# Kernel tuning notes

Measured on AMD Instinct MI355X. Metric: run time of the kernel, lower is better.

Reference implementation:

```python
import jax, jax.numpy as jnp
import numpy as np

D = 2        # NUM_DIM (spatial/velocity dimension)
B = 64       # number of (r, r') query pairs
P = 512      # num coefficient positions
NV = 64      # num velocity quadrature points
NC = 1       # num coefficient channels (sigma)
H = 64       # attention MLP hidden width
TW = 128     # transport MLP width
DEPTH = 3    # res_block_depth


def setup_inputs() -> dict:
    key = jax.random.key(0)
    ks = jax.random.split(key, 20)
    rnd = lambda i, shape, s=1.0: (s * jax.random.normal(ks[i], shape, dtype=jnp.float32))
    uni = lambda i, shape: jax.random.uniform(ks[i], shape, dtype=jnp.float32)
    return dict(
        coords=rnd(0, (B, 2 * D)),
        coords_prime=rnd(1, (B, 2 * D)),
        scattering_kernel=uni(2, (B, NV)),
        position_coords=rnd(3, (P, D)),
        sigma=uni(4, (P, NC)),
        velocity_coords=rnd(5, (NV, D)),
        velocity_weights=uni(6, (NV,)),
        self_scattering_kernel=uni(7, (NV, NV)),
        aW0=rnd(8, (2 * D + 2, H), (2 * D + 2) ** -0.5), ab0=jnp.zeros((H,), jnp.float32),
        aW1=rnd(9, (H, H), H ** -0.5), ab1=jnp.zeros((H,), jnp.float32),
        aW2=rnd(10, (H, 1), H ** -0.5), ab2=jnp.zeros((1,), jnp.float32),
        tW0=rnd(11, (4 * D + NC, TW), (4 * D + NC) ** -0.5), tb0=jnp.zeros((TW,), jnp.float32),
        tW1=rnd(12, (TW, TW), TW ** -0.5), tb1=jnp.zeros((TW,), jnp.float32),
        tW2=rnd(13, (TW, TW), TW ** -0.5), tb2=jnp.zeros((TW,), jnp.float32),
        rW=rnd(14, (DEPTH - 1, TW, TW), TW ** -0.5), rb=jnp.zeros((DEPTH - 1, TW), jnp.float32),
        fW=rnd(15, (TW, 1), TW ** -0.5), fb=jnp.zeros((1,), jnp.float32),
    )


def _coeff(x, v, pos, vals, aW0, ab0, aW1, ab1, aW2, ab2):
    # x, v: (..., D); pos: (P, D); vals: (P, NC)
    coords = jnp.concatenate([x, v], axis=-1)                          # (..., 2D)
    ang_g = v / jnp.sqrt(jnp.sum(v * v, axis=-1, keepdims=True) + 1e-16)
    rel = x[..., None, :] - pos                                        # (..., P, D)
    rd = jnp.sqrt(jnp.sum(rel * rel, axis=-1) + 1e-16)                 # (..., P)
    pl = jnp.einsum('...pd,...d->...p', rel, ang_g)                    # positions_local
    al = pl / (rd + 1e-8)                                              # angles_local
    frames = jnp.stack([al, pl], axis=-1)                              # (..., P, 2)
    q = jnp.broadcast_to(coords[..., None, :], frames.shape[:-1] + (coords.shape[-1],))
    qk = jnp.concatenate([q, frames], axis=-1)                         # (..., P, 2D+2)
    h = jax.nn.relu(qk @ aW0 + ab0)
    h = jax.nn.relu(h @ aW1 + ab1)
    logits = (h @ aW2 + ab2)[..., 0]                                   # (..., P)
    logits = jnp.where(pl > 0, logits, -1e30)
    attw = jax.nn.softmax(logits, axis=-1)
    attn = jnp.einsum('...p,pc->...c', attw, vals)                     # (..., NC)
    return jnp.exp(-attn)


def _transport(x, v, xp, vp, pos, vals,
               aW0, ab0, aW1, ab1, aW2, ab2, tW0, tb0, tW1, tb1, tW2, tb2):
    coeff = _coeff(x, v, pos, vals, aW0, ab0, aW1, ab1, aW2, ab2)
    inp = jnp.concatenate([x, v, xp, vp, coeff], axis=-1)              # (..., 4D+NC)
    h = jax.nn.relu(inp @ tW0 + tb0)
    h = jax.nn.relu(h @ tW1 + tb1)
    h = jax.nn.relu(h @ tW2 + tb2)                                     # activate_final=True
    return jnp.exp(h)                                                  # (..., TW)


def _forward(coords, coords_prime, scattering_kernel, position_coords, sigma,
             velocity_coords, velocity_weights, self_scattering_kernel,
             aW0, ab0, aW1, ab1, aW2, ab2, tW0, tb0, tW1, tb1, tW2, tb2,
             rW, rb, fW, fb):
    x, v = coords[:, :D], coords[:, D:]
    xp, vp = coords_prime[:, :D], coords_prime[:, D:]
    mlp_p = (aW0, ab0, aW1, ab1, aW2, ab2, tW0, tb0, tW1, tb1, tW2, tb2)
    # direct transport term: (B, TW)
    g = _transport(x, v, xp, vp, position_coords, sigma, *mlp_p)
    # scatter model: vmap over velocity_coords -> (B, NV, TW)
    b = coords.shape[0]
    vB = jnp.broadcast_to(velocity_coords, (b, NV, D))
    xB = jnp.broadcast_to(x[:, None, :], (b, NV, D))
    xpB = jnp.broadcast_to(xp[:, None, :], (b, NV, D))
    vpB = jnp.broadcast_to(vp[:, None, :], (b, NV, D))
    cur = _transport(xB, vB, xpB, vpB, position_coords, sigma, *mlp_p)
    res_w = (1.0 - self_scattering_kernel) * velocity_weights          # (NV, NV)
    outs = [cur]
    for l in range(DEPTH - 1):  # layer_stack with per-layer params
        r = jnp.einsum('ij,bjw->biw', res_w, cur)
        r = jax.nn.relu(r @ rW[l] + rb[l])                             # MLP([TW]), activate_final
        cur = cur + r
        outs.append(cur)
    scat = jnp.stack(outs)                                             # (DEPTH, B, NV, TW)
    w = (1.0 - scattering_kernel) * velocity_weights                   # (B, NV)
    g = g + jnp.einsum('bj,dbjw->bw', w, scat)
    return g @ fW + fb                                                 # (B, 1)


def reference(coords, coords_prime, scattering_kernel, position_coords, sigma,
              velocity_coords, velocity_weights, self_scattering_kernel,
              aW0, ab0, aW1, ab1, aW2, ab2, tW0, tb0, tW1, tb1, tW2, tb2,
              rW, rb, fW, fb):
    return _forward(coords, coords_prime, scattering_kernel, position_coords, sigma,
                    velocity_coords, velocity_weights, self_scattering_kernel,
                    aW0, ab0, aW1, ab1, aW2, ab2, tW0, tb0, tW1, tb1, tW2, tb2,
                    rW, rb, fW, fb)
```

## Files before the change

kernel.cpp:

```cpp
#include <hip/hip_runtime.h>
#include <hip/hip_bf16.h>
#include <math.h>

#define D 2
#define B 64
#define P 512
#define NV 64
#define H 64
#define TW 128
#define NQ (B*NV + B)

typedef short short8 __attribute__((ext_vector_type(8)));
typedef short short4v __attribute__((ext_vector_type(4)));
typedef float f32x4 __attribute__((ext_vector_type(4)));
typedef int   int4v  __attribute__((ext_vector_type(4)));

static __device__ __forceinline__ unsigned short f2bf(float f) {
    unsigned int u = __builtin_bit_cast(unsigned int, f);
    u += 0x7FFFu + ((u >> 16) & 1u);
    return (unsigned short)(u >> 16);
}
static __device__ __forceinline__ unsigned int pk2bf(float a, float b) {
    __hip_bfloat162 h = __float22bfloat162_rn(make_float2(a, b));
    unsigned int u;
    __builtin_memcpy(&u, &h, 4);
    return u;
}

__global__ __launch_bounds__(256, 2) void coeff_kernel(
    const float* __restrict__ coords, const float* __restrict__ vel,
    const float* __restrict__ pos, const float* __restrict__ sigma,
    const float* __restrict__ aW0, const float* __restrict__ ab0,
    const float* __restrict__ aW1, const float* __restrict__ ab1,
    const float* __restrict__ aW2, const float* __restrict__ ab2,
    float* __restrict__ coeff_out)
{
    __shared__ unsigned short s_w1t[64*72];
    __shared__ float2 s_pos[P];
    __shared__ float  s_logit[2*P];

    const int tid  = threadIdx.x;
    const int lane = tid & 63, wid = tid >> 6;
    const int l15 = lane & 15, lg = lane >> 4;
    const int qi   = wid >> 1;
    const int half = wid & 1;
    const int q = blockIdx.x*2 + qi;

    for (int i = tid; i < H*H; i += 256) {
        const int k = i >> 6, n = i & 63;
        s_w1t[n*72 + k] = f2bf(aW1[i]);
    }
    {
        const float4 p4 = ((const float4*)pos)[tid];
        *(float4*)&s_pos[tid*2] = p4;
    }

    float x0, x1, v0, v1;
    {
        int b;
        if (q < B*NV) { b = q >> 6; const int j = q & 63;
            v0 = vel[2*j]; v1 = vel[2*j+1];
        } else { b = q - B*NV;
            v0 = coords[4*b+2]; v1 = coords[4*b+3];
        }
        x0 = coords[4*b]; x1 = coords[4*b+1];
    }
    const float rinv = rsqrtf(v0*v0 + v1*v1 + 1e-16f);
    const float a0 = v0*rinv, a1 = v1*rinv;

    float basev[16], w4v[16], w5v[16];
    #pragma unroll
    for (int jj = 0; jj < 16; ++jj) {
        const int k = lg*8 + (jj & 7) + (jj >> 3)*32;
        basev[jj] = ab0[k] + x0*aW0[k] + x1*aW0[64+k] + v0*aW0[128+k] + v1*aW0[192+k];
        w4v[jj]   = aW0[256+k];
        w5v[jj]   = aW0[320+k];
    }

    f32x4 b1v[4], w2v[4];
    #pragma unroll
    for (int nt = 0; nt < 4; ++nt) {
        const int n0 = nt*16 + lg*4;
        b1v[nt] = *(const f32x4*)&ab1[n0];
        w2v[nt] = *(const f32x4*)&aW2[n0];
    }
    __syncthreads();

    short8 afrag[4][2];
    #pragma unroll
    for (int nt = 0; nt < 4; ++nt)
        #pragma unroll
        for (int ks = 0; ks < 2; ++ks)
            afrag[nt][ks] = *(const short8*)&s_w1t[(nt*16 + l15)*72 + ks*32 + lg*8];

    #pragma unroll
    for (int jj = 0; jj < 16; ++jj)
        asm volatile("" : "+v"(basev[jj]), "+v"(w4v[jj]), "+v"(w5v[jj]));
    #pragma unroll
    for (int nt = 0; nt < 4; ++nt)
        asm volatile("" : "+v"(b1v[nt]), "+v"(w2v[nt]),
                          "+v"(afrag[nt][0]), "+v"(afrag[nt][1]));

    float2 pxy = s_pos[half*256 + l15];
    for (int ps = 0; ps < 16; ++ps) {
        const int prow = half*256 + ps*16 + l15;
        const float2 nxt = (ps < 15) ? s_pos[prow + 16] : pxy;

        const float rx = x0 - pxy.x;
        const float ry = x1 - pxy.y;
        const float rd = __builtin_amdgcn_sqrtf(rx*rx + ry*ry + 1e-16f);
        const float pl = rx*a0 + ry*a1;
        const float al = __fdividef(pl, rd + 1e-8f);

        int4v wlo, whi;
        #pragma unroll
        for (int jp = 0; jp < 4; ++jp) {
            const float t0 = fmaxf(fmaf(pl, w5v[2*jp],   fmaf(al, w4v[2*jp],   basev[2*jp])),   0.f);
            const float t1 = fmaxf(fmaf(pl, w5v[2*jp+1], fmaf(al, w4v[2*jp+1], basev[2*jp+1])), 0.f);
            const float u0 = fmaxf(fmaf(pl, w5v[8+2*jp],   fmaf(al, w4v[8+2*jp],   basev[8+2*jp])),   0.f);
            const float u1 = fmaxf(fmaf(pl, w5v[8+2*jp+1], fmaf(al, w4v[8+2*jp+1], basev[8+2*jp+1])), 0.f);
            wlo[jp] = (int)pk2bf(t0, t1);
            whi[jp] = (int)pk2bf(u0, u1);
        }
        const short8 bf0 = __builtin_bit_cast(short8, wlo);
        const short8 bf1 = __builtin_bit_cast(short8, whi);

        float ssum = 0.f;
        #pragma unroll
        for (int nt = 0; nt < 4; ++nt) {
            f32x4 acc = b1v[nt];
            acc = __builtin_amdgcn_mfma_f32_16x16x32_bf16(afrag[nt][0], bf0, acc, 0, 0, 0);
            acc = __builtin_amdgcn_mfma_f32_16x16x32_bf16(afrag[nt][1], bf1, acc, 0, 0, 0);
            ssum += fmaxf(acc[0], 0.f) * w2v[nt][0];
            ssum += fmaxf(acc[1], 0.f) * w2v[nt][1];
            ssum += fmaxf(acc[2], 0.f) * w2v[nt][2];
            ssum += fmaxf(acc[3], 0.f) * w2v[nt][3];
        }
        ssum += __shfl_xor(ssum, 16, 64);
        ssum += __shfl_xor(ssum, 32, 64);
        if (lane < 16) s_logit[qi*512 + prow] = (pl > 0.f) ? ssum : -1e30f;
        pxy = nxt;
    }
    __syncthreads();

    const float* lgb = &s_logit[qi*512];
    const float4 l0 = *(const float4*)&lgb[lane*8];
    const float4 l1 = *(const float4*)&lgb[lane*8 + 4];
    float m = fmaxf(fmaxf(fmaxf(l0.x, l0.y), fmaxf(l0.z, l0.w)),
                    fmaxf(fmaxf(l1.x, l1.y), fmaxf(l1.z, l1.w)));
    #pragma unroll
    for (int o = 32; o > 0; o >>= 1) m = fmaxf(m, __shfl_xor(m, o, 64));

    const float4 g0 = *(const float4*)&sigma[lane*8];
    const float4 g1 = *(const float4*)&sigma[lane*8 + 4];
    float S = 0.f, T = 0.f, e;
    e = __expf(l0.x - m); S += e; T += e*g0.x;
    e = __expf(l0.y - m); S += e; T += e*g0.y;
    e = __expf(l0.z - m); S += e; T += e*g0.z;
    e = __expf(l0.w - m); S += e; T += e*g0.w;
    e = __expf(l1.x - m); S += e; T += e*g1.x;
    e = __expf(l1.y - m); S += e; T += e*g1.y;
    e = __expf(l1.z - m); S += e; T += e*g1.z;
    e = __expf(l1.w - m); S += e; T += e*g1.w;
    #pragma unroll
    for (int o = 32; o > 0; o >>= 1) { S += __shfl_xor(S, o, 64); T += __shfl_xor(T, o, 64); }
    if (lane == 0 && half == 0) coeff_out[q] = __expf(-(T / S));
}

__global__ __launch_bounds__(128) void transport_kernel(
    const float* __restrict__ coords, const float* __restrict__ coordsp,
    const float* __restrict__ vel,
    const float* __restrict__ tW0, const float* __restrict__ tb0,
    const float* __restrict__ tW1, const float* __restrict__ tb1,
    const float* __restrict__ tW2, const float* __restrict__ tb2,
    const float* __restrict__ coeff_ws, float* __restrict__ cur_ws,
    float* __restrict__ g_ws)
{
    __shared__ float sh[TW];
    const int t = threadIdx.x, q = blockIdx.x;
    float in2, in3;
    int b;
    if (q < B*NV) { b = q >> 6; const int j = q & 63;
        in2 = vel[2*j]; in3 = vel[2*j+1];
    } else { b = q - B*NV;
        in2 = coords[4*b+2]; in3 = coords[4*b+3];
    }
    const float in0 = coords[4*b],  in1 = coords[4*b+1];
    const float p0 = coordsp[4*b],  p1 = coordsp[4*b+1];
    const float p2 = coordsp[4*b+2], p3 = coordsp[4*b+3];
    const float cf = coeff_ws[q];

    float h = tb0[t]
        + in0*tW0[t]       + in1*tW0[TW+t]   + in2*tW0[2*TW+t] + in3*tW0[3*TW+t]
        + p0 *tW0[4*TW+t]  + p1 *tW0[5*TW+t] + p2 *tW0[6*TW+t] + p3 *tW0[7*TW+t]
        + cf *tW0[8*TW+t];
    h = fmaxf(h, 0.f);
    sh[t] = h; __syncthreads();

    float h2 = tb1[t];
    for (int i = 0; i < TW; ++i) h2 += sh[i]*tW1[i*TW+t];
    h2 = fmaxf(h2, 0.f);
    __syncthreads(); sh[t] = h2; __syncthreads();

    float h3 = tb2[t];
    for (int i = 0; i < TW; ++i) h3 += sh[i]*tW2[i*TW+t];
    h3 = fmaxf(h3, 0.f);
    const float o = expf(h3);

    if (q < B*NV) cur_ws[q*TW + t] = o;
    else          g_ws[(q - B*NV)*TW + t] = o;
}

__global__ __launch_bounds__(512) void scatter_kernel(
    const float* __restrict__ scat_k, const float* __restrict__ vw,
    const float* __restrict__ ssk,
    const float* __restrict__ rW, const float* __restrict__ rb,
    const float* __restrict__ fW, const float* __restrict__ fb,
    const float* __restrict__ cur_ws, const float* __restrict__ g_ws,
    float* __restrict__ out)
{
    __shared__ unsigned short s_At[128*72];
    __shared__ unsigned short s_r[64*136];
    __shared__ unsigned short s_rWt[128*136];
    __shared__ float s_wl[NV];
    __shared__ float s_fin[4*128];
    __shared__ float s_red[2];

    const int tid = threadIdx.x, b = blockIdx.x;
    const int lane = tid & 63, wid = tid >> 6;
    const int wm = wid & 3, wn = wid >> 2;
    const int l15 = lane & 15, lg = lane >> 4;
    const int irow = wm*16 + lg*4;

    if (tid < NV) s_wl[tid] = (1.f - scat_k[b*NV + tid]) * vw[tid];

    {
        const int w = tid & 127, j0 = tid >> 7;
        #pragma unroll
        for (int k = 0; k < 16; ++k) {
            const int j = j0 + 4*k;
            s_At[w*72 + j] = f2bf(cur_ws[(b*NV + j)*TW + w]);
        }
    }

    float areg[4][4], sreg[4][4];
    #pragma unroll
    for (int n = 0; n < 4; ++n) {
        const int wcol = wn*64 + n*16 + l15;
        #pragma unroll
        for (int rg = 0; rg < 4; ++rg) {
            const float v = cur_ws[(b*NV + irow + rg)*TW + wcol];
            areg[n][rg] = v; sreg[n][rg] = v;
        }
    }

    for (int l = 0; l < 2; ++l) {
        {
            const float* rWl = rW + l*TW*TW;
            const int w = tid & 127, u0 = (tid >> 7)*4;
            #pragma unroll
            for (int k = 0; k < 8; ++k) {
                const int u = u0 + 16*k;
                short4v pk;
                #pragma unroll
                for (int c = 0; c < 4; ++c) pk[c] = (short)f2bf(rWl[(u+c)*TW + w]);
                *(short4v*)&s_rWt[w*136 + u] = pk;
            }
        }
        __syncthreads();

        {
            short8 afrag[2];
            const int row = wm*16 + l15;
            #pragma unroll
            for (int ks = 0; ks < 2; ++ks) {
                const int k0 = ks*32 + lg*8;
                #pragma unroll
                for (int j = 0; j < 8; ++j) {
                    const float rv = (1.f - ssk[row*NV + k0 + j]) * vw[k0 + j];
                    afrag[ks][j] = (short)f2bf(rv);
                }
            }
            #pragma unroll
            for (int n = 0; n < 4; ++n) {
                const int col = wn*64 + n*16 + l15;
                f32x4 acc = {0.f, 0.f, 0.f, 0.f};
                #pragma unroll
                for (int ks = 0; ks < 2; ++ks) {
                    const short8 bfr = *(const short8*)&s_At[col*72 + ks*32 + lg*8];
                    acc = __builtin_amdgcn_mfma_f32_16x16x32_bf16(afrag[ks], bfr, acc, 0, 0, 0);
                }
                #pragma unroll
                for (int rg = 0; rg < 4; ++rg)
                    s_r[(irow + rg)*136 + col] = f2bf(acc[rg]);
            }
        }
        __syncthreads();

        {
            short8 af2[4];
            #pragma unroll
            for (int ks = 0; ks < 4; ++ks)
                af2[ks] = *(const short8*)&s_r[(wm*16 + l15)*136 + ks*32 + lg*8];
            #pragma unroll
            for (int n = 0; n < 4; ++n) {
                const int col = wn*64 + n*16 + l15;
                f32x4 acc = {0.f, 0.f, 0.f, 0.f};
                #pragma unroll
                for (int ks = 0; ks < 4; ++ks) {
                    const short8 bfr = *(const short8*)&s_rWt[col*136 + ks*32 + lg*8];
                    acc = __builtin_amdgcn_mfma_f32_16x16x32_bf16(af2[ks], bfr, acc, 0, 0, 0);
                }
                const float rbv = rb[l*TW + col];
                short4v pk;
                #pragma unroll
                for (int rg = 0; rg < 4; ++rg) {
                    areg[n][rg] += fmaxf(acc[rg] + rbv, 0.f);
                    sreg[n][rg] += areg[n][rg];
                    pk[rg] = (short)f2bf(areg[n][rg]);
                }
                *(short4v*)&s_At[col*72 + irow] = pk;
            }
        }
        __syncthreads();
    }

    float p[4];
    #pragma unroll
    for (int n = 0; n < 4; ++n) {
        float acc = 0.f;
        #pragma unroll
        for (int rg = 0; rg < 4; ++rg) acc += s_wl[irow + rg] * sreg[n][rg];
        acc += __shfl_xor(acc, 16, 64);
        acc += __shfl_xor(acc, 32, 64);
        p[n] = acc;
    }
    if (lg == 0) {
        #pragma unroll
        for (int n = 0; n < 4; ++n)
            s_fin[wm*128 + wn*64 + n*16 + l15] = p[n];
    }
    __syncthreads();

    if (tid < 128) {
        const int w = tid;
        const float tot = s_fin[w] + s_fin[128 + w] + s_fin[256 + w] + s_fin[384 + w];
        float pw = (g_ws[b*TW + w] + tot) * fW[w];
        #pragma unroll
        for (int o = 32; o > 0; o >>= 1) pw += __shfl_down(pw, o, 64);
        if ((tid & 63) == 0) s_red[tid >> 6] = pw;
    }
    __syncthreads();
    if (tid == 0) out[b] = s_red[0] + s_red[1] + fb[0];
}

extern "C" void kernel_launch(void* const* d_in, const int* in_sizes, int n_in,
                              void* d_out, int out_size, void* d_ws, size_t ws_size,
                              hipStream_t stream) {
    const float* coords  = (const float*)d_in[0];
    const float* coordsp = (const float*)d_in[1];
    const float* scatk   = (const float*)d_in[2];
    const float* pos     = (const float*)d_in[3];
    const float* sigma   = (const float*)d_in[4];
    const float* vel     = (const float*)d_in[5];
    const float* vw      = (const float*)d_in[6];
    const float* ssk     = (const float*)d_in[7];
    const float* aW0 = (const float*)d_in[8];
    const float* ab0 = (const float*)d_in[9];
    const float* aW1 = (const float*)d_in[10];
    const float* ab1 = (const float*)d_in[11];
    const float* aW2 = (const float*)d_in[12];
    const float* ab2 = (const float*)d_in[13];
    const float* tW0 = (const float*)d_in[14];
    const float* tb0 = (const float*)d_in[15];
    const float* tW1 = (const float*)d_in[16];
    const float* tb1 = (const float*)d_in[17];
    const float* tW2 = (const float*)d_in[18];
    const float* tb2 = (const float*)d_in[19];
    const float* rW  = (const float*)d_in[20];
    const float* rb  = (const float*)d_in[21];
    const float* fW  = (const float*)d_in[22];
    const float* fb  = (const float*)d_in[23];
    float* out = (float*)d_out;

    float* ws = (float*)d_ws;
    float* coeff_ws = ws;
    float* cur_ws   = ws + 4224;
    float* g_ws     = cur_ws + B*NV*TW;

    hipLaunchKernelGGL(coeff_kernel, dim3(NQ/2), dim3(256), 0, stream,
        coords, vel, pos, sigma, aW0, ab0, aW1, ab1, aW2, ab2, coeff_ws);
    hipLaunchKernelGGL(transport_kernel, dim3(NQ), dim3(128), 0, stream,
        coords, coordsp, vel, tW0, tb0, tW1, tb1, tW2, tb2, coeff_ws, cur_ws, g_ws);
    hipLaunchKernelGGL(scatter_kernel, dim3(B), dim3(512), 0, stream,
        scatk, vw, ssk, rW, rb, fW, fb, cur_ws, g_ws, out);
}
```

Measured before the change: 80.79 us.

## Compute first attention MLP layer with MFMA and stage activations via LDS

```diff
diff --git a/kernel.cpp b/kernel.cpp
--- a/kernel.cpp
+++ b/kernel.cpp
@@ -38,6 +38,7 @@
     __shared__ unsigned short s_w1t[64*72];
     __shared__ float2 s_pos[P];
     __shared__ float  s_logit[2*P];
+    __shared__ unsigned int s_h1[4*16*36];
 
     const int tid  = threadIdx.x;
     const int lane = tid & 63, wid = tid >> 6;
@@ -68,13 +69,25 @@
     const float rinv = rsqrtf(v0*v0 + v1*v1 + 1e-16f);
     const float a0 = v0*rinv, a1 = v1*rinv;
 
-    float basev[16], w4v[16], w5v[16];
-    #pragma unroll
-    for (int jj = 0; jj < 16; ++jj) {
-        const int k = lg*8 + (jj & 7) + (jj >> 3)*32;
-        basev[jj] = ab0[k] + x0*aW0[k] + x1*aW0[64+k] + v0*aW0[128+k] + v1*aW0[192+k];
-        w4v[jj]   = aW0[256+k];
-        w5v[jj]   = aW0[320+k];
+    int4v af1i[4];
+    #pragma unroll
+    for (int t = 0; t < 4; ++t) {
+        int4v v = {0, 0, 0, 0};
+        if (lg == 0) {
+            const int n = 16*t + l15;
+            v[0] = (int)pk2bf(aW0[256 + n], aW0[320 + n]);
+        }
+        af1i[t] = v;
+    }
+
+    f32x4 basec[4];
+    #pragma unroll
+    for (int t = 0; t < 4; ++t) {
+        #pragma unroll
+        for (int r = 0; r < 4; ++r) {
+            const int k = 16*t + 4*lg + r;
+            basec[t][r] = ab0[k] + x0*aW0[k] + x1*aW0[64+k] + v0*aW0[128+k] + v1*aW0[192+k];
+        }
     }
 
     f32x4 b1v[4], w2v[4];
@@ -94,12 +107,12 @@
             afrag[nt][ks] = *(const short8*)&s_w1t[(nt*16 + l15)*72 + ks*32 + lg*8];
 
     #pragma unroll
-    for (int jj = 0; jj < 16; ++jj)
-        asm volatile("" : "+v"(basev[jj]), "+v"(w4v[jj]), "+v"(w5v[jj]));
-    #pragma unroll
     for (int nt = 0; nt < 4; ++nt)
-        asm volatile("" : "+v"(b1v[nt]), "+v"(w2v[nt]),
-                          "+v"(afrag[nt][0]), "+v"(afrag[nt][1]));
+        asm volatile("" : "+v"(b1v[nt]), "+v"(w2v[nt]), "+v"(basec[nt]),
+                          "+v"(af1i[nt]), "+v"(afrag[nt][0]), "+v"(afrag[nt][1]));
+
+    const unsigned int woff = (wid*16 + l15)*36;
+    unsigned int* __restrict__ h1row = &s_h1[woff];
 
     float2 pxy = s_pos[half*256 + l15];
     for (int ps = 0; ps < 16; ++ps) {
@@ -112,25 +125,29 @@
         const float pl = rx*a0 + ry*a1;
         const float al = __fdividef(pl, rd + 1e-8f);
 
-        int4v wlo, whi;
-        #pragma unroll
-        for (int jp = 0; jp < 4; ++jp) {
-            const float t0 = fmaxf(fmaf(pl, w5v[2*jp],   fmaf(al, w4v[2*jp],   basev[2*jp])),   0.f);
-            const float t1 = fmaxf(fmaf(pl, w5v[2*jp+1], fmaf(al, w4v[2*jp+1], basev[2*jp+1])), 0.f);
-            const float u0 = fmaxf(fmaf(pl, w5v[8+2*jp],   fmaf(al, w4v[8+2*jp],   basev[8+2*jp])),   0.f);
-            const float u1 = fmaxf(fmaf(pl, w5v[8+2*jp+1], fmaf(al, w4v[8+2*jp+1], basev[8+2*jp+1])), 0.f);
-            wlo[jp] = (int)pk2bf(t0, t1);
-            whi[jp] = (int)pk2bf(u0, u1);
-        }
-        const short8 bf0 = __builtin_bit_cast(short8, wlo);
-        const short8 bf1 = __builtin_bit_cast(short8, whi);
+        int4v b1i = {0, 0, 0, 0};
+        b1i[0] = (lg == 0) ? (int)pk2bf(al, pl) : 0;
+        const short8 bf1_ = __builtin_bit_cast(short8, b1i);
+
+        #pragma unroll
+        for (int t = 0; t < 4; ++t) {
+            f32x4 acc = basec[t];
+            acc = __builtin_amdgcn_mfma_f32_16x16x32_bf16(
+                      __builtin_bit_cast(short8, af1i[t]), bf1_, acc, 0, 0, 0);
+            const unsigned int p0 = pk2bf(fmaxf(acc[0], 0.f), fmaxf(acc[1], 0.f));
+            const unsigned int p1 = pk2bf(fmaxf(acc[2], 0.f), fmaxf(acc[3], 0.f));
+            *(uint2*)&h1row[8*t + 2*lg] = make_uint2(p0, p1);
+        }
+
+        const short8 bf2a = *(const short8*)&h1row[4*lg];
+        const short8 bf2b = *(const short8*)&h1row[16 + 4*lg];
 
         float ssum = 0.f;
         #pragma unroll
         for (int nt = 0; nt < 4; ++nt) {
             f32x4 acc = b1v[nt];
-            acc = __builtin_amdgcn_mfma_f32_16x16x32_bf16(afrag[nt][0], bf0, acc, 0, 0, 0);
-            acc = __builtin_amdgcn_mfma_f32_16x16x32_bf16(afrag[nt][1], bf1, acc, 0, 0, 0);
+            acc = __builtin_amdgcn_mfma_f32_16x16x32_bf16(afrag[nt][0], bf2a, acc, 0, 0, 0);
+            acc = __builtin_amdgcn_mfma_f32_16x16x32_bf16(afrag[nt][1], bf2b, acc, 0, 0, 0);
             ssum += fmaxf(acc[0], 0.f) * w2v[nt][0];
             ssum += fmaxf(acc[1], 0.f) * w2v[nt][1];
             ssum += fmaxf(acc[2], 0.f) * w2v[nt][2];
```

Measured after the change: 84.12 us. +4.1%, slower.

## Batch transport MLP into 64-query tiles using bf16 MFMA

Applied to the files above, without the earlier changes.

```diff
diff --git a/kernel.cpp b/kernel.cpp
--- a/kernel.cpp
+++ b/kernel.cpp
@@ -101,16 +101,24 @@
         asm volatile("" : "+v"(b1v[nt]), "+v"(w2v[nt]),
                           "+v"(afrag[nt][0]), "+v"(afrag[nt][1]));
 
-    float2 pxy = s_pos[half*256 + l15];
+    float pl, al;
+    {
+        const float2 p0v = s_pos[half*256 + l15];
+        const float rx = x0 - p0v.x, ry = x1 - p0v.y;
+        const float rd = __builtin_amdgcn_sqrtf(rx*rx + ry*ry + 1e-16f);
+        pl = rx*a0 + ry*a1;
+        al = __fdividef(pl, rd + 1e-8f);
+    }
     for (int ps = 0; ps < 16; ++ps) {
         const int prow = half*256 + ps*16 + l15;
-        const float2 nxt = (ps < 15) ? s_pos[prow + 16] : pxy;
-
-        const float rx = x0 - pxy.x;
-        const float ry = x1 - pxy.y;
-        const float rd = __builtin_amdgcn_sqrtf(rx*rx + ry*ry + 1e-16f);
-        const float pl = rx*a0 + ry*a1;
-        const float al = __fdividef(pl, rd + 1e-8f);
+        float pln = pl, aln = al;
+        if (ps < 15) {
+            const float2 nxt = s_pos[prow + 16];
+            const float rxn = x0 - nxt.x, ryn = x1 - nxt.y;
+            const float rdn = __builtin_amdgcn_sqrtf(rxn*rxn + ryn*ryn + 1e-16f);
+            pln = rxn*a0 + ryn*a1;
+            aln = __fdividef(pln, rdn + 1e-8f);
+        }
 
         int4v wlo, whi;
         #pragma unroll
@@ -139,7 +147,7 @@
         ssum += __shfl_xor(ssum, 16, 64);
         ssum += __shfl_xor(ssum, 32, 64);
         if (lane < 16) s_logit[qi*512 + prow] = (pl > 0.f) ? ssum : -1e30f;
-        pxy = nxt;
+        pl = pln; al = aln;
     }
     __syncthreads();
 
@@ -167,7 +175,7 @@
     if (lane == 0 && half == 0) coeff_out[q] = __expf(-(T / S));
 }
 
-__global__ __launch_bounds__(128) void transport_kernel(
+__global__ __launch_bounds__(512) void transport_kernel(
     const float* __restrict__ coords, const float* __restrict__ coordsp,
     const float* __restrict__ vel,
     const float* __restrict__ tW0, const float* __restrict__ tb0,
@@ -176,39 +184,131 @@
     const float* __restrict__ coeff_ws, float* __restrict__ cur_ws,
     float* __restrict__ g_ws)
 {
-    __shared__ float sh[TW];
-    const int t = threadIdx.x, q = blockIdx.x;
-    float in2, in3;
-    int b;
-    if (q < B*NV) { b = q >> 6; const int j = q & 63;
-        in2 = vel[2*j]; in3 = vel[2*j+1];
-    } else { b = q - B*NV;
-        in2 = coords[4*b+2]; in3 = coords[4*b+3];
-    }
-    const float in0 = coords[4*b],  in1 = coords[4*b+1];
-    const float p0 = coordsp[4*b],  p1 = coordsp[4*b+1];
-    const float p2 = coordsp[4*b+2], p3 = coordsp[4*b+3];
-    const float cf = coeff_ws[q];
-
-    float h = tb0[t]
-        + in0*tW0[t]       + in1*tW0[TW+t]   + in2*tW0[2*TW+t] + in3*tW0[3*TW+t]
-        + p0 *tW0[4*TW+t]  + p1 *tW0[5*TW+t] + p2 *tW0[6*TW+t] + p3 *tW0[7*TW+t]
-        + cf *tW0[8*TW+t];
-    h = fmaxf(h, 0.f);
-    sh[t] = h; __syncthreads();
-
-    float h2 = tb1[t];
-    for (int i = 0; i < TW; ++i) h2 += sh[i]*tW1[i*TW+t];
-    h2 = fmaxf(h2, 0.f);
-    __syncthreads(); sh[t] = h2; __syncthreads();
-
-    float h3 = tb2[t];
-    for (int i = 0; i < TW; ++i) h3 += sh[i]*tW2[i*TW+t];
-    h3 = fmaxf(h3, 0.f);
-    const float o = expf(h3);
-
-    if (q < B*NV) cur_ws[q*TW + t] = o;
-    else          g_ws[(q - B*NV)*TW + t] = o;
+    __shared__ unsigned short s_w0t[128*40];
+    __shared__ unsigned short s_wt[128*136];
+    __shared__ unsigned short s_in[64*40];
+    __shared__ unsigned short s_ha[64*136];
+    __shared__ unsigned short s_hb[64*136];
+    __shared__ float s_b[3*128];
+
+    const int tid = threadIdx.x, g = blockIdx.x;
+    const int lane = tid & 63, wid = tid >> 6;
+    const int wm = wid & 3, wn = wid >> 2;
+    const int l15 = lane & 15, lg = lane >> 4;
+    const int irow = wm*16 + lg*4;
+    const int qbase = g*64;
+
+    for (int i = tid; i < 128*40; i += 512) {
+        const int t = i / 40, k = i % 40;
+        s_w0t[i] = (k < 9) ? f2bf(tW0[k*TW + t]) : 0;
+    }
+    for (int i = tid; i < 64*40; i += 512) s_in[i] = 0;
+    {
+        const int n = tid & 127, u0 = (tid >> 7)*4;
+        #pragma unroll
+        for (int k8 = 0; k8 < 8; ++k8) {
+            const int u = u0 + 16*k8;
+            short4v pk;
+            #pragma unroll
+            for (int c = 0; c < 4; ++c) pk[c] = (short)f2bf(tW1[(u+c)*TW + n]);
+            *(short4v*)&s_wt[n*136 + u] = pk;
+        }
+    }
+    if (tid < 128) { s_b[tid] = tb0[tid]; s_b[128+tid] = tb1[tid]; s_b[256+tid] = tb2[tid]; }
+    __syncthreads();
+
+    if (tid < 64) {
+        const int q = qbase + tid;
+        int b; float v0, v1;
+        if (q < B*NV) { b = q >> 6; const int j = q & 63;
+            v0 = vel[2*j]; v1 = vel[2*j+1];
+        } else { b = q - B*NV;
+            v0 = coords[4*b+2]; v1 = coords[4*b+3];
+        }
+        unsigned short* r = &s_in[tid*40];
+        r[0] = f2bf(coords[4*b]);   r[1] = f2bf(coords[4*b+1]);
+        r[2] = f2bf(v0);            r[3] = f2bf(v1);
+        r[4] = f2bf(coordsp[4*b]);  r[5] = f2bf(coordsp[4*b+1]);
+        r[6] = f2bf(coordsp[4*b+2]);r[7] = f2bf(coordsp[4*b+3]);
+        r[8] = f2bf(coeff_ws[q]);
+    }
+    __syncthreads();
+
+    {
+        const short8 a0 = *(const short8*)&s_in[(wm*16 + l15)*40 + lg*8];
+        #pragma unroll
+        for (int nt = 0; nt < 4; ++nt) {
+            const int col = wn*64 + nt*16 + l15;
+            const short8 b0f = *(const short8*)&s_w0t[col*40 + lg*8];
+            const float bias = s_b[col];
+            f32x4 acc = { bias, bias, bias, bias };
+            acc = __builtin_amdgcn_mfma_f32_16x16x32_bf16(a0, b0f, acc, 0, 0, 0);
+            #pragma unroll
+            for (int rg = 0; rg < 4; ++rg)
+                s_ha[(irow + rg)*136 + col] = f2bf(fmaxf(acc[rg], 0.f));
+        }
+    }
+    __syncthreads();
+
+    {
+        short8 af[4];
+        #pragma unroll
+        for (int ks = 0; ks < 4; ++ks)
+            af[ks] = *(const short8*)&s_ha[(wm*16 + l15)*136 + ks*32 + lg*8];
+        #pragma unroll
+        for (int nt = 0; nt < 4; ++nt) {
+            const int col = wn*64 + nt*16 + l15;
+            const float bias = s_b[128 + col];
+            f32x4 acc = { bias, bias, bias, bias };
+            #pragma unroll
+            for (int ks = 0; ks < 4; ++ks) {
+                const short8 bfr = *(const short8*)&s_wt[col*136 + ks*32 + lg*8];
+                acc = __builtin_amdgcn_mfma_f32_16x16x32_bf16(af[ks], bfr, acc, 0, 0, 0);
+            }
+            #pragma unroll
+            for (int rg = 0; rg < 4; ++rg)
+                s_hb[(irow + rg)*136 + col] = f2bf(fmaxf(acc[rg], 0.f));
+        }
+    }
+    __syncthreads();
+
+    {
+        const int n = tid & 127, u0 = (tid >> 7)*4;
+        #pragma unroll
+        for (int k8 = 0; k8 < 8; ++k8) {
+            const int u = u0 + 16*k8;
+            short4v pk;
+            #pragma unroll
+            for (int c = 0; c < 4; ++c) pk[c] = (short)f2bf(tW2[(u+c)*TW + n]);
+            *(short4v*)&s_wt[n*136 + u] = pk;
+        }
+    }
+    __syncthreads();
+
+    {
+        short8 af[4];
+        #pragma unroll
+        for (int ks = 0; ks < 4; ++ks)
+            af[ks] = *(const short8*)&s_hb[(wm*16 + l15)*136 + ks*32 + lg*8];
+        #pragma unroll
+        for (int nt = 0; nt < 4; ++nt) {
+            const int col = wn*64 + nt*16 + l15;
+            const float bias = s_b[256 + col];
+            f32x4 acc = { bias, bias, bias, bias };
+            #pragma unroll
+            for (int ks = 0; ks < 4; ++ks) {
+                const short8 bfr = *(const short8*)&s_wt[col*136 + ks*32 + lg*8];
+                acc = __builtin_amdgcn_mfma_f32_16x16x32_bf16(af[ks], bfr, acc, 0, 0, 0);
+            }
+            #pragma unroll
+            for (int rg = 0; rg < 4; ++rg) {
+                const float o = __expf(fmaxf(acc[rg], 0.f));
+                const int q = qbase + irow + rg;
+                if (q < B*NV) cur_ws[q*TW + col] = o;
+                else          g_ws[(q - B*NV)*TW + col] = o;
+            }
+        }
+    }
 }
 
 __global__ __launch_bounds__(512) void scatter_kernel(
@@ -390,7 +490,7 @@
 
     hipLaunchKernelGGL(coeff_kernel, dim3(NQ/2), dim3(256), 0, stream,
         coords, vel, pos, sigma, aW0, ab0, aW1, ab1, aW2, ab2, coeff_ws);
-    hipLaunchKernelGGL(transport_kernel, dim3(NQ), dim3(128), 0, stream,
+    hipLaunchKernelGGL(transport_kernel, dim3(NQ/64), dim3(512), 0, stream,
         coords, coordsp, vel, tW0, tb0, tW1, tb1, tW2, tb2, coeff_ws, cur_ws, g_ws);
     hipLaunchKernelGGL(scatter_kernel, dim3(B), dim3(512), 0, stream,
         scatk, vw, ssk, rW, rb, fW, fb, cur_ws, g_ws, out);
```

After: 69.56 us. 1.16x faster.
